# Optimization experiments

Measured on AMD Instinct MI355X. Metric: run time of the kernel, lower is better.

## Reference

```python
import jax, jax.numpy as jnp
import numpy as np

N = 128000      # total nodes
B = 128         # graphs, 1000 nodes each
L = 4           # max_levels
S_MAX = 1000    # max cluster size (<= PositionalEncoding max_len)
H = 128         # hidden dim (all conv output dims equal)
IN_DIM = 128
OUT_DIM = 1
E = 1024000
TEMP = 0.1


def layer_norm(x, g, b, eps=1e-5):
    mu = jnp.mean(x, axis=-1, keepdims=True)
    v = jnp.mean((x - mu) ** 2, axis=-1, keepdims=True)
    return (x - mu) * jax.lax.rsqrt(v + eps) * g + b


def transformer_conv(x, src, dst, Wq, bq, Wk, bk, Wv, bv, Ws, bs):
    # PyG TransformerConv, heads=1: softmax over in-edges of each dst node
    q = x @ Wq + bq
    k = x @ Wk + bk
    v = x @ Wv + bv
    logits = jnp.sum(q[dst] * k[src], axis=-1) / jnp.sqrt(jnp.float32(q.shape[-1]))
    m = jax.ops.segment_max(logits, dst, num_segments=N)
    e = jnp.exp(logits - m[dst])
    s = jax.ops.segment_sum(e, dst, num_segments=N)
    alpha = e / s[dst]
    agg = jax.ops.segment_sum(alpha[:, None] * v[src], dst, num_segments=N)
    return agg + x @ Ws + bs  # root_weight skip connection


def pos_encoding(S, d):
    pos = jnp.arange(S, dtype=jnp.float32)[:, None]
    div = jnp.exp(jnp.arange(0, d, 2, dtype=jnp.float32) * (-jnp.log(10000.0) / d))
    pe = jnp.zeros((S, d), jnp.float32)
    pe = pe.at[:, 0::2].set(jnp.sin(pos * div))
    pe = pe.at[:, 1::2].set(jnp.cos(pos * div))
    return pe


def gru(xseq, Wih, Whh, bih, bhh):
    # xseq: [G, S, H] -> outputs [G, S, H]; torch GRU gate math
    G = xseq.shape[0]
    def step(h, x_t):
        gi = x_t @ Wih.T + bih
        gh = h @ Whh.T + bhh
        ir, iz, inn = jnp.split(gi, 3, axis=-1)
        hr, hz, hn = jnp.split(gh, 3, axis=-1)
        r = jax.nn.sigmoid(ir + hr)
        z = jax.nn.sigmoid(iz + hz)
        n = jnp.tanh(inn + r * hn)
        h_new = (1.0 - z) * n + z * h
        return h_new, h_new
    h0 = jnp.zeros((G, Whh.shape[1]), xseq.dtype)
    _, outs = jax.lax.scan(step, h0, jnp.swapaxes(xseq, 0, 1))
    return jnp.swapaxes(outs, 0, 1)


def _forward(x, tree_edge_index, call_sequences, batch,
             conv_Wq, conv_bq, conv_Wk, conv_bk, conv_Wv, conv_bv, conv_Ws, conv_bs,
             ln_g, ln_b, centers, proj_W, proj_b,
             gru_Wih, gru_Whh, gru_bih, gru_bhh, seqln_g, seqln_b,
             lin1_W, lin1_b, lin2_W, lin2_b):
    src, dst = tree_edge_index[0], tree_edge_index[1]
    h = x
    for i in range(3):  # conv1/bn1, conv2/bn2, conv4/bn4
        h = transformer_conv(h, src, dst, conv_Wq[i], conv_bq[i], conv_Wk[i],
                             conv_bk[i], conv_Wv[i], conv_bv[i], conv_Ws[i], conv_bs[i])
        h = jax.nn.relu(layer_norm(h, ln_g[i], ln_b[i]))

    # HierarchicalClassifier: cosine-sim soft assignment + center variance loss
    xn = h / jnp.maximum(jnp.linalg.norm(h, axis=-1, keepdims=True), 1e-8)
    cn = centers / jnp.maximum(jnp.linalg.norm(centers, axis=-1, keepdims=True), 1e-8)
    assign = jax.nn.softmax((xn @ cn.T) / TEMP, axis=-1)
    level_ids = jnp.argmax(assign, axis=1).astype(jnp.int32)
    iu0, iu1 = np.triu_indices(L, k=1)
    dvec = jnp.linalg.norm(centers[iu0] - centers[iu1], axis=-1)
    distance = -jnp.var(dvec, ddof=1)  # torch.var is unbiased

    # ragged gather + pad: group nodes by (graph, cluster), sort by call order
    G = B * L
    group = batch * L + level_ids                       # [N]
    order = jnp.argsort(group * N + call_sequences)     # sort by group, then call
    g_sorted = group[order]
    counts = jax.ops.segment_sum(jnp.ones((N,), jnp.int32), group, num_segments=G)
    starts = jnp.cumsum(counts) - counts
    pos = jnp.arange(N, dtype=jnp.int32) - starts[g_sorted]
    seq = jnp.zeros((G, S_MAX, H), h.dtype).at[g_sorted, pos].set(h[order])

    # SequentialRNN: proj -> pos-enc -> GRU -> LayerNorm -> ReLU (mask unused)
    sin = seq @ proj_W + proj_b + pos_encoding(S_MAX, H)[None]
    outs = gru(sin, gru_Wih, gru_Whh, gru_bih, gru_bhh)
    outs = jax.nn.relu(layer_norm(outs, seqln_g, seqln_b))

    # scatter valid positions back; singleton clusters keep raw features
    node_out = jnp.zeros_like(h).at[order].set(outs[g_sorted, pos])
    singleton = (counts[group] == 1)
    gout = jnp.where(singleton[:, None], h, node_out)

    y = jax.nn.gelu(gout @ lin1_W + lin1_b, approximate=False)
    y = jax.nn.sigmoid(y @ lin2_W + lin2_b)
    return y, distance


def setup_inputs():
    key = jax.random.key(0)
    ks = jax.random.split(key, 16)
    p = lambda k, s: jax.random.normal(k, s, jnp.float32) * 0.02
    return {
        "x": jax.random.normal(ks[0], (N, IN_DIM), jnp.float32),
        "tree_edge_index": jax.random.randint(ks[1], (2, E), 0, N, dtype=jnp.int32),
        "call_sequences": jax.random.permutation(ks[2], N).astype(jnp.int32),
        "batch": (jnp.arange(N, dtype=jnp.int32) * B) // N,  # 1000 nodes per graph
        "conv_Wq": p(ks[3], (3, H, H)), "conv_bq": jnp.zeros((3, H), jnp.float32),
        "conv_Wk": p(ks[4], (3, H, H)), "conv_bk": jnp.zeros((3, H), jnp.float32),
        "conv_Wv": p(ks[5], (3, H, H)), "conv_bv": jnp.zeros((3, H), jnp.float32),
        "conv_Ws": p(ks[6], (3, H, H)), "conv_bs": jnp.zeros((3, H), jnp.float32),
        "ln_g": jnp.ones((3, H), jnp.float32), "ln_b": jnp.zeros((3, H), jnp.float32),
        "centers": jax.random.normal(ks[7], (L, H), jnp.float32),
        "proj_W": p(ks[8], (H, H)), "proj_b": jnp.zeros((H,), jnp.float32),
        "gru_Wih": p(ks[9], (3 * H, H)), "gru_Whh": p(ks[10], (3 * H, H)),
        "gru_bih": jnp.zeros((3 * H,), jnp.float32), "gru_bhh": jnp.zeros((3 * H,), jnp.float32),
        "seqln_g": jnp.ones((H,), jnp.float32), "seqln_b": jnp.zeros((H,), jnp.float32),
        "lin1_W": p(ks[11], (H, 8)), "lin1_b": jnp.zeros((8,), jnp.float32),
        "lin2_W": p(ks[12], (8, OUT_DIM)), "lin2_b": jnp.zeros((OUT_DIM,), jnp.float32),
    }


def reference(x, tree_edge_index, call_sequences, batch,
              conv_Wq, conv_bq, conv_Wk, conv_bk, conv_Wv, conv_bv, conv_Ws, conv_bs,
              ln_g, ln_b, centers, proj_W, proj_b,
              gru_Wih, gru_Whh, gru_bih, gru_bhh, seqln_g, seqln_b,
              lin1_W, lin1_b, lin2_W, lin2_b):
    return _forward(x, tree_edge_index, call_sequences, batch,
                    conv_Wq, conv_bq, conv_Wk, conv_bk, conv_Wv, conv_bv, conv_Ws, conv_bs,
                    ln_g, ln_b, centers, proj_W, proj_b,
                    gru_Wih, gru_Whh, gru_bih, gru_bhh, seqln_g, seqln_b,
                    lin1_W, lin1_b, lin2_W, lin2_b)
```

## Files before the change

kernel.cpp:

```cpp
#include <hip/hip_runtime.h>

#define NN 128000
#define EE 1024000
#define HH 128
#define GG 512
#define SMAX 1000
#define NCHUNK 500

typedef unsigned int u32;
typedef unsigned short u16;

constexpr size_t NH     = (size_t)NN*HH;
constexpr size_t F_H    = 0;
constexpr size_t F_A    = NH;
constexpr size_t F_B    = 2*NH;
constexpr size_t F_NODE = F_A + (size_t)NN*192;
constexpr size_t F_CN   = 3*NH;
constexpr size_t F_WKT  = F_CN   + 512;
constexpr size_t F_WQK  = F_WKT  + 3*16384;
constexpr size_t F_BQK  = F_WQK  + 3*16384;
constexpr size_t F_CW   = F_BQK  + 3*128;
constexpr size_t F_PEW  = F_CW   + 128*384;
constexpr size_t F_PEB  = F_PEW  + 1000*384;
constexpr size_t F_END  = F_PEB  + 1000*128;

constexpr size_t I_ROWP = 0;
constexpr size_t I_CUR  = I_ROWP + NN + 8;
constexpr size_t I_COL  = I_CUR  + NN;
constexpr size_t I_GRP  = I_COL  + EE;
constexpr size_t I_INV  = I_GRP  + NN;
constexpr size_t I_POS  = I_INV  + NN;
constexpr size_t I_GN   = I_POS  + NN;
constexpr size_t I_CNT  = I_GN   + (size_t)GG*SMAX;
constexpr size_t I_CH   = I_CNT  + GG;
constexpr size_t I_BS   = I_CH   + (size_t)NCHUNK*GG;
constexpr size_t I_WT   = I_BS   + 512;
constexpr size_t I_END  = I_WT   + 64*384;

constexpr size_t WS_NEEDED = F_END*4 + I_END*4;

__device__ inline float wredf(float v){
  #pragma unroll
  for (int o = 32; o; o >>= 1) v += __shfl_xor(v, o);
  return v;
}
__device__ inline u32 bf16rne(float f){
  u32 u = __float_as_uint(f);
  return (u + 0x7fffu + ((u >> 16) & 1u)) >> 16;
}
__device__ inline float bf2f(u16 u){
  return __uint_as_float(((u32)u) << 16);
}
__device__ inline float frcp(float x){
#if __has_builtin(__builtin_amdgcn_rcpf)
  return __builtin_amdgcn_rcpf(x);
#else
  return 1.f / x;
#endif
}

typedef _Float16 h2_t __attribute__((ext_vector_type(2)));
__device__ inline float dot2f(u32 w, u32 h, float acc){
#if __has_builtin(__builtin_amdgcn_fdot2)
  return __builtin_amdgcn_fdot2(__builtin_bit_cast(h2_t, w),
                                __builtin_bit_cast(h2_t, h), acc, false);
#else
  float r;
  asm("v_dot2_f32_f16 %0, %1, %2, %3" : "=v"(r) : "v"(w), "v"(h), "v"(acc));
  return r;
#endif
}
#define PIN4(v) asm volatile("" : "+v"((v).x), "+v"((v).y), "+v"((v).z), "+v"((v).w))

__global__ void k_sentinel(float* __restrict__ out, int n, float val){
  int i = blockIdx.x * 256 + threadIdx.x;
  if (i < n) out[i] = val;
}

__global__ void k_zero(int* __restrict__ p){
  p[blockIdx.x * 256 + threadIdx.x] = 0;
}
__global__ void k_hist(const int* __restrict__ dst, int* __restrict__ deg){
  int e = blockIdx.x * 256 + threadIdx.x;
  atomicAdd(&deg[dst[e]], 1);
}
__global__ void k_s1(const int* __restrict__ deg, int* __restrict__ bsum){
  __shared__ int red[256];
  int t = threadIdx.x;
  red[t] = deg[blockIdx.x * 256 + t];
  __syncthreads();
  for (int s = 128; s; s >>= 1){ if (t < s) red[t] += red[t + s]; __syncthreads(); }
  if (!t) bsum[blockIdx.x] = red[0];
}
__global__ void k_s2(int* __restrict__ bsum){
  __shared__ int arr[512];
  int t = threadIdx.x;
  int v0 = (t < NCHUNK) ? bsum[t] : 0;
  arr[t] = v0; __syncthreads();
  for (int off = 1; off < 512; off <<= 1){
    int v = (t >= off) ? arr[t - off] : 0;
    __syncthreads();
    arr[t] += v;
    __syncthreads();
  }
  if (t < NCHUNK) bsum[t] = arr[t] - v0;
}
__global__ void k_s3(const int* __restrict__ bsum, int* __restrict__ row_ptr,
                     int* __restrict__ cursor){
  __shared__ int arr[256];
  int t = threadIdx.x;
  int i = blockIdx.x * 256 + t;
  int v0 = cursor[i];
  arr[t] = v0; __syncthreads();
  for (int off = 1; off < 256; off <<= 1){
    int v = (t >= off) ? arr[t - off] : 0;
    __syncthreads();
    arr[t] += v;
    __syncthreads();
  }
  int exc = arr[t] - v0 + bsum[blockIdx.x];
  row_ptr[i] = exc;
  cursor[i]  = exc;
  if (i == 0) row_ptr[NN] = EE;
}
__global__ void k_scatter(const int* __restrict__ src, const int* __restrict__ dst,
                          int* __restrict__ cursor, int* __restrict__ col){
  int e = blockIdx.x * 256 + threadIdx.x;
  int idx = atomicAdd(&cursor[dst[e]], 1);
  col[idx] = src[e];
}

__global__ void k_setup(const float* __restrict__ centers, float* __restrict__ cn,
                        float* __restrict__ dist_out){
  __shared__ float red[128];
  int t = threadIdx.x;
  for (int l = 0; l < 4; ++l){
    float v = centers[l*128 + t];
    red[t] = v * v; __syncthreads();
    for (int s = 64; s; s >>= 1){ if (t < s) red[t] += red[t + s]; __syncthreads(); }
    float nrm = sqrtf(red[0]);
    __syncthreads();
    cn[l*128 + t] = v / fmaxf(nrm, 1e-8f);
  }
  const int iu0[6] = {0,0,0,1,1,2}, iu1[6] = {1,2,3,2,3,3};
  __shared__ float dv[6];
  for (int p = 0; p < 6; ++p){
    float d = centers[iu0[p]*128 + t] - centers[iu1[p]*128 + t];
    red[t] = d * d; __syncthreads();
    for (int s = 64; s; s >>= 1){ if (t < s) red[t] += red[t + s]; __syncthreads(); }
    if (!t) dv[p] = sqrtf(red[0]);
    __syncthreads();
  }
  if (!t){
    float mean = 0.f;
    for (int p = 0; p < 6; ++p) mean += dv[p];
    mean /= 6.f;
    float var = 0.f;
    for (int p = 0; p < 6; ++p){ float d = dv[p] - mean; var += d * d; }
    var /= 5.f;
    dist_out[0] = -var;
  }
}

__global__ void k_pe(const float* __restrict__ projb, float* __restrict__ peb){
  int p = blockIdx.x, t = threadIdx.x;
  float ex  = (float)(t >> 1) * (-2.0f * 9.210340371976184f / 128.0f);
  float ang = (float)p * expf(ex);
  float v = (t & 1) ? cosf(ang) : sinf(ang);
  peb[p*128 + t] = v + projb[t];
}
__global__ void k_pew(const float* __restrict__ peb, const float* __restrict__ Wih,
                      const float* __restrict__ bih, float* __restrict__ pew){
  int p = blockIdx.x;
  int j = blockIdx.y * 128 + threadIdx.x;
  const float* pb = peb + p*128;
  const float* wr = Wih + (size_t)j*128;
  float acc = bih[j];
  #pragma unroll 4
  for (int m = 0; m < 128; ++m) acc += pb[m] * wr[m];
  pew[(size_t)p*384 + j] = acc;
}
__global__ void k_combw(const float* __restrict__ projW, const float* __restrict__ Wih,
                        float* __restrict__ cw){
  int kk = blockIdx.x;
  int j  = blockIdx.y * 128 + threadIdx.x;
  const float* pr = projW + (size_t)kk*128;
  const float* wr = Wih + (size_t)j*128;
  float acc = 0.f;
  #pragma unroll 4
  for (int m = 0; m < 128; ++m) acc += pr[m] * wr[m];
  cw[(size_t)kk*384 + j] = acc;
}
__global__ void k_tr(const float* __restrict__ Wk, float* __restrict__ wkt){
  int kk = blockIdx.x, l = blockIdx.y, c = threadIdx.x;
  wkt[(size_t)l*16384 + kk*128 + c] = Wk[(size_t)l*16384 + c*128 + kk];
}
__global__ void k_mv(const float* __restrict__ M, const float* __restrict__ v,
                     float* __restrict__ out){
  int l = blockIdx.x, i = threadIdx.x;
  const float* row = M + (size_t)l*16384 + (size_t)i*128;
  const float* vv = v + l*128;
  float acc = 0.f;
  #pragma unroll 4
  for (int j = 0; j < 128; ++j) acc += row[j] * vv[j];
  out[l*128 + i] = acc;
}
__global__ void k_packwhh16(const float* __restrict__ Whh, u32* __restrict__ wt){
  int kp = blockIdx.x;
  int j  = blockIdx.y * 128 + threadIdx.x;
  _Float16 a = (_Float16)Whh[(size_t)j*128 + 2*kp];
  _Float16 b = (_Float16)Whh[(size_t)j*128 + 2*kp + 1];
  u32 lo = (u32)__builtin_bit_cast(u16, a);
  u32 hi = (u32)__builtin_bit_cast(u16, b);
  wt[(size_t)j*64 + kp] = (hi << 16) | lo;
}

__global__ __launch_bounds__(256, 2) void k_gemm(
    const float* __restrict__ X, const float* __restrict__ W, int ldw,
    const float* __restrict__ X2, const float* __restrict__ W2,
    const float* __restrict__ bias, const float* __restrict__ pew,
    const int* __restrict__ pos, float* __restrict__ out,
    u16* __restrict__ outb, int ldo,
    const float* __restrict__ lng, const float* __restrict__ lnb,
    const float* __restrict__ bvv, const int* __restrict__ rowp){
  __shared__ __align__(16) float Wl[64*132];
  __shared__ __align__(16) float Xl[64*132];
  int tid = threadIdx.x;
  int rb = blockIdx.x * 128;
  int cb = blockIdx.y * 128;
  int rg = tid >> 4;
  int cg = tid & 15;
  int kxor = (cg >> 2) & 3;
  float acc[8][8];
  #pragma unroll
  for (int a = 0; a < 8; ++a)
    #pragma unroll
    for (int b = 0; b < 8; ++b) acc[a][b] = 0.f;
  int nhalf = X2 ? 4 : 2;
  for (int half = 0; half < nhalf; ++half){
    const float* Xs = (half < 2) ? X : X2;
    const float* Ws = (half < 2) ? W : W2;
    int ldws = (half < 2) ? ldw : 128;
    int hk = half & 1;
    __syncthreads();
    #pragma unroll
    for (int it = 0; it < 8; ++it){
      int idx = it*256 + tid;
      int kk = idx >> 5, c4 = idx & 31;
      *(float4*)&Wl[kk*132 + c4*4] =
          *(const float4*)&Ws[(size_t)(hk*64 + kk)*ldws + cb + c4*4];
    }
    #pragma unroll
    for (int it = 0; it < 8; ++it){
      int idx = it*256 + tid;
      int r = idx >> 4, c4 = idx & 15;
      float4 xv = *(const float4*)&Xs[(size_t)(rb + r)*128 + hk*64 + c4*4];
      Xl[(c4*4+0)*132 + r] = xv.x;
      Xl[(c4*4+1)*132 + r] = xv.y;
      Xl[(c4*4+2)*132 + r] = xv.z;
      Xl[(c4*4+3)*132 + r] = xv.w;
    }
    __syncthreads();
    #pragma unroll 2
    for (int kk = 0; kk < 64; ++kk){
      int kx = kk ^ kxor;
      float4 wa = *(const float4*)&Wl[kx*132 + cg*8];
      float4 wb = *(const float4*)&Wl[kx*132 + cg*8 + 4];
      float4 xa = *(const float4*)&Xl[kx*132 + rg*8];
      float4 xb = *(const float4*)&Xl[kx*132 + rg*8 + 4];
      float xs[8] = {xa.x, xa.y, xa.z, xa.w, xb.x, xb.y, xb.z, xb.w};
      float ws[8] = {wa.x, wa.y, wa.z, wa.w, wb.x, wb.y, wb.z, wb.w};
      #pragma unroll
      for (int rr = 0; rr < 8; ++rr)
        #pragma unroll
        for (int j = 0; j < 8; ++j) acc[rr][j] += xs[rr] * ws[j];
    }
  }
  if (lng){
    float gv[8], bl[8], bb[8], vv[8];
    #pragma unroll
    for (int j = 0; j < 8; ++j){
      int c = cg*8 + j;
      gv[j] = lng[c]; bl[j] = lnb[c]; bb[j] = bias[c]; vv[j] = bvv[c];
    }
    #pragma unroll
    for (int rr = 0; rr < 8; ++rr){
      int r = rb + rg*8 + rr;
      bool deg = rowp[r+1] > rowp[r];
      float rs = 0.f, rq = 0.f;
      #pragma unroll
      for (int j = 0; j < 8; ++j){
        float v = acc[rr][j] + bb[j] + (deg ? vv[j] : 0.f);
        acc[rr][j] = v;
        rs += v; rq += v*v;
      }
      #pragma unroll
      for (int o = 8; o; o >>= 1){ rs += __shfl_xor(rs, o); rq += __shfl_xor(rq, o); }
      float mu = rs * 0.0078125f;
      float var = rq * 0.0078125f - mu*mu;
      float rstd = rsqrtf(var + 1e-5f);
      float ov[8];
      #pragma unroll
      for (int j = 0; j < 8; ++j)
        ov[j] = fmaxf((acc[rr][j] - mu)*rstd*gv[j] + bl[j], 0.f);
      float* op = out + (size_t)r*128 + cg*8;
      *(float4*)op       = *(const float4*)&ov[0];
      *(float4*)(op + 4) = *(const float4*)&ov[4];
    }
    return;
  }
  #pragma unroll
  for (int rr = 0; rr < 8; ++rr){
    int r = rb + rg*8 + rr;
    float bv[8];
    if (pos){
      const float* pw = pew + (size_t)pos[r]*384 + cb + cg*8;
      #pragma unroll
      for (int j = 0; j < 8; ++j) bv[j] = pw[j];
    } else if (bias){
      #pragma unroll
      for (int j = 0; j < 8; ++j) bv[j] = bias[cb + cg*8 + j];
    } else {
      #pragma unroll
      for (int j = 0; j < 8; ++j) bv[j] = 0.f;
    }
    if (outb){
      u16 ob[8];
      #pragma unroll
      for (int j = 0; j < 8; ++j) ob[j] = (u16)bf16rne(acc[rr][j] + bv[j]);
      *(uint4*)(outb + (size_t)r*ldo + cb + cg*8) = *(const uint4*)ob;
    } else {
      float ov[8];
      #pragma unroll
      for (int j = 0; j < 8; ++j) ov[j] = acc[rr][j] + bv[j];
      float* op = out + (size_t)r*ldo + cb + cg*8;
      *(float4*)op       = *(const float4*)&ov[0];
      *(float4*)(op + 4) = *(const float4*)&ov[4];
    }
  }
}

__global__ __launch_bounds__(256) void k_edge(
    const float* __restrict__ qt, const float* __restrict__ xsrc,
    const int* __restrict__ row_ptr, const int* __restrict__ col,
    float* __restrict__ xagg){
  int d = blockIdx.x * 8 + (threadIdx.x >> 5);
  int lane = threadIdx.x & 31;
  int e0 = row_ptr[d], e1 = row_ptr[d+1];
  if (e0 == e1){
    *(float4*)&xagg[(size_t)d*128 + lane*4] = make_float4(0.f, 0.f, 0.f, 0.f);
    return;
  }
  const float S = 0.08838834764831845f;
  float4 qv = *(const float4*)&qt[(size_t)d*128 + lane*4];
  float ss0 = 0.f, ss1 = 0.f;
  float4 A0 = make_float4(0.f,0.f,0.f,0.f), A1 = make_float4(0.f,0.f,0.f,0.f);
  int e = e0;
  for (; e + 1 < e1; e += 2){
    float4 x0 = *(const float4*)&xsrc[(size_t)col[e]  *128 + lane*4];
    float4 x1 = *(const float4*)&xsrc[(size_t)col[e+1]*128 + lane*4];
    float p0 = qv.x*x0.x + qv.y*x0.y + qv.z*x0.z + qv.w*x0.w;
    float p1 = qv.x*x1.x + qv.y*x1.y + qv.z*x1.z + qv.w*x1.w;
    #pragma unroll
    for (int o = 16; o; o >>= 1){ p0 += __shfl_xor(p0, o); p1 += __shfl_xor(p1, o); }
    float el0 = __expf(p0 * S);
    float el1 = __expf(p1 * S);
    ss0 += el0; ss1 += el1;
    A0.x += el0*x0.x; A0.y += el0*x0.y; A0.z += el0*x0.z; A0.w += el0*x0.w;
    A1.x += el1*x1.x; A1.y += el1*x1.y; A1.z += el1*x1.z; A1.w += el1*x1.w;
  }
  if (e < e1){
    float4 x0 = *(const float4*)&xsrc[(size_t)col[e]*128 + lane*4];
    float p0 = qv.x*x0.x + qv.y*x0.y + qv.z*x0.z + qv.w*x0.w;
    #pragma unroll
    for (int o = 16; o; o >>= 1) p0 += __shfl_xor(p0, o);
    float el0 = __expf(p0 * S);
    ss0 += el0;
    A0.x += el0*x0.x; A0.y += el0*x0.y; A0.z += el0*x0.z; A0.w += el0*x0.w;
  }
  float inv = 1.f / (ss0 + ss1);
  *(float4*)&xagg[(size_t)d*128 + lane*4] =
      make_float4((A0.x+A1.x)*inv, (A0.y+A1.y)*inv, (A0.z+A1.z)*inv, (A0.w+A1.w)*inv);
}

__global__ __launch_bounds__(256) void k_lnrelu_cls(
    const float* __restrict__ in, const float* __restrict__ g,
    const float* __restrict__ b, const float* __restrict__ bvv,
    const int* __restrict__ rowp, float* __restrict__ outp,
    const float* __restrict__ cn, const int* __restrict__ batch,
    const int* __restrict__ callsq, int* __restrict__ grp, int* __restrict__ inv){
  int node = blockIdx.x * 4 + (threadIdx.x >> 6);
  int lane = threadIdx.x & 63;
  float x0 = in[(size_t)node*128 + 2*lane], x1 = in[(size_t)node*128 + 2*lane + 1];
  if (rowp[node+1] > rowp[node]){
    x0 += bvv[2*lane];
    x1 += bvv[2*lane + 1];
  }
  float s = wredf(x0 + x1);
  float qq = wredf(x0*x0 + x1*x1);
  float mu = s * 0.0078125f;
  float var = qq * 0.0078125f - mu*mu;
  float rstd = rsqrtf(var + 1e-5f);
  float y0 = fmaxf((x0 - mu)*rstd*g[2*lane]   + b[2*lane],   0.f);
  float y1 = fmaxf((x1 - mu)*rstd*g[2*lane+1] + b[2*lane+1], 0.f);
  outp[(size_t)node*128 + 2*lane]     = y0;
  outp[(size_t)node*128 + 2*lane + 1] = y1;
  float p0 = y0*cn[      2*lane] + y1*cn[      2*lane+1];
  float p1 = y0*cn[128 + 2*lane] + y1*cn[128 + 2*lane+1];
  float p2 = y0*cn[256 + 2*lane] + y1*cn[256 + 2*lane+1];
  float p3 = y0*cn[384 + 2*lane] + y1*cn[384 + 2*lane+1];
  p0 = wredf(p0); p1 = wredf(p1); p2 = wredf(p2); p3 = wredf(p3);
  if (lane == 0){
    float best = p0; int bi = 0;
    if (p1 > best){ best = p1; bi = 1; }
    if (p2 > best){ best = p2; bi = 2; }
    if (p3 > best){ best = p3; bi = 3; }
    grp[node] = batch[node]*4 + bi;
    inv[callsq[node]] = node;
  }
}

__global__ __launch_bounds__(256) void k_g1(const int* __restrict__ inv,
                                            const int* __restrict__ grp,
                                            int* __restrict__ ch){
  __shared__ int hist[GG];
  int c = blockIdx.x, t = threadIdx.x;
  hist[t] = 0; hist[t + 256] = 0;
  __syncthreads();
  int g = grp[inv[c*256 + t]];
  atomicAdd(&hist[g], 1);
  __syncthreads();
  ch[c*GG + t] = hist[t];
  ch[c*GG + 256 + t] = hist[256 + t];
}
__global__ void k_g2(int* __restrict__ ch, int* __restrict__ cnt){
  __shared__ int arr[512];
  int g = blockIdx.x, t = threadIdx.x;
  int v0 = (t < NCHUNK) ? ch[(size_t)t*GG + g] : 0;
  arr[t] = v0; __syncthreads();
  for (int off = 1; off < 512; off <<= 1){
    int v = (t >= off) ? arr[t - off] : 0;
    __syncthreads();
    arr[t] += v;
    __syncthreads();
  }
  if (t < NCHUNK) ch[(size_t)t*GG + g] = arr[t] - v0;
  if (t == 511) cnt[g] = arr[511];
}
__global__ __launch_bounds__(256) void k_g3(
    const int* __restrict__ inv, const int* __restrict__ grp,
    const int* __restrict__ ch, int* __restrict__ pos, int* __restrict__ gn){
  __shared__ int hist[GG];
  int c = blockIdx.x, t = threadIdx.x;
  hist[t] = 0; hist[t + 256] = 0;
  __syncthreads();
  int node = inv[c*256 + t];
  int g = grp[node];
  int lane = t & 63, w = t >> 6;
  int before = 0, total = 0;
  for (int j = 0; j < 64; ++j){
    int gj = __shfl(g, j);
    if (gj == g){ total++; if (j < lane) before++; }
  }
  int base = 0;
  for (int wv = 0; wv < 4; ++wv){
    if (w == wv){
      base = hist[g];
      if (before == total - 1) hist[g] = base + total;
    }
    __syncthreads();
  }
  int p = ch[c*GG + g] + base + before;
  pos[node] = p;
  gn[(size_t)g*SMAX + p] = node;
}

#define GRU_STEP(XR, XZ, XN, NODE, CUR, NXT)                                     \
  {                                                                              \
    const uint4* HB = (const uint4*)&hb16[CUR][0];                               \
    uint4 hh[8];                                                                 \
    _Pragma("unroll")                                                            \
    for (int s = 0; s < 8; ++s) hh[s] = HB[kh*8 + s];                            \
    __builtin_amdgcn_s_setprio(1);                                               \
    float ar = 0.f, az = 0.f, an = 0.f;                                          \
    _Pragma("unroll")                                                            \
    for (int s = 0; s < 8; ++s){                                                 \
      ar = dot2f(wr_[s].x, hh[s].x, ar); az = dot2f(wz_[s].x, hh[s].x, az); an = dot2f(wn_[s].x, hh[s].x, an); \
      ar = dot2f(wr_[s].y, hh[s].y, ar); az = dot2f(wz_[s].y, hh[s].y, az); an = dot2f(wn_[s].y, hh[s].y, an); \
      ar = dot2f(wr_[s].z, hh[s].z, ar); az = dot2f(wz_[s].z, hh[s].z, az); an = dot2f(wn_[s].z, hh[s].z, an); \
      ar = dot2f(wr_[s].w, hh[s].w, ar); az = dot2f(wz_[s].w, hh[s].w, az); an = dot2f(wn_[s].w, hh[s].w, an); \
    }                                                                            \
    ar += __shfl_xor(ar, 1); az += __shfl_xor(az, 1); an += __shfl_xor(an, 1);   \
    ar += br; az += bz; an += bn;                                                \
    float er = __expf(-((XR) + ar));                                             \
    float rg_ = frcp(1.f + er);                                                  \
    float ez = __expf(-((XZ) + az));                                             \
    float zg_ = frcp(1.f + ez);                                                  \
    float yv = (XN) + rg_ * an;                                                  \
    float e2 = __expf(-2.f * yv);                                                \
    float ng_ = (1.f - e2) * frcp(1.f + e2);                                     \
    float hnew = ng_ + zg_ * (hprev - ng_);                                      \
    __builtin_amdgcn_s_setprio(0);                                               \
    hprev = hnew;                                                                \
    u16 hbf = (u16)bf16rne(hnew);                                                \
    u32 pk = ((u32)(u16)__shfl_xor((int)hbf, 2) << 16) | (u32)hbf;               \
    if (!kh){                                                                    \
      _Float16 hf16 = (_Float16)hnew;                                            \
      hb16[NXT][j] = __builtin_bit_cast(u16, hf16);                              \
    }                                                                            \
    if ((t & 3) == 0)                                                            \
      *(u32*)(node_out + (size_t)(NODE)*128 + j) = pk;                           \
    asm volatile("s_waitcnt lgkmcnt(0)" ::: "memory");                           \
    __builtin_amdgcn_s_barrier();                                                \
    asm volatile("" ::: "memory");                                               \
  }

__global__ __launch_bounds__(256)
__attribute__((amdgpu_waves_per_eu(2, 2)))
void k_gru(
    const u16* __restrict__ gi, const u32* __restrict__ wt,
    const float* __restrict__ bhh, const int* __restrict__ gn,
    const int* __restrict__ cnt, u16* __restrict__ node_out){
  __shared__ __align__(16) u16 hb16[2][128];
  int t = threadIdx.x;
  int j = t >> 1;
  int kh = t & 1;
  int g = blockIdx.x;
  int my = cnt[g];
  if (my <= 1) return;
  uint4 wr_[8], wz_[8], wn_[8];
  {
    const uint4* wt4 = (const uint4*)wt;
    size_t b0 = (size_t)(0*128 + j)*16 + kh*8;
    size_t b1 = (size_t)(1*128 + j)*16 + kh*8;
    size_t b2 = (size_t)(2*128 + j)*16 + kh*8;
    #pragma unroll
    for (int s = 0; s < 8; ++s){
      wr_[s] = wt4[b0 + s];
      wz_[s] = wt4[b1 + s];
      wn_[s] = wt4[b2 + s];
    }
    #pragma unroll
    for (int s = 0; s < 8; ++s){
      PIN4(wr_[s]); PIN4(wz_[s]); PIN4(wn_[s]);
    }
  }
  if (t < 128) hb16[0][t] = 0;
  float br = bhh[j], bz = bhh[128 + j], bn = bhh[256 + j];
  const int* gnr = gn + (size_t)g*SMAX;
  float hprev = 0.f;
  int n0 = gnr[0];
  int n1 = gnr[min(1, my - 1)];
  int n2 = gnr[min(2, my - 1)];
  int n3 = gnr[min(3, my - 1)];
  u16 a0r, a0z, a0n, a1r, a1z, a1n;
  u16 b0r, b0z, b0n, b1r, b1z, b1n;
  {
    const u16* g0 = gi + (size_t)n0*384;
    const u16* g1 = gi + (size_t)n1*384;
    a0r = g0[j]; a0z = g0[128 + j]; a0n = g0[256 + j];
    a1r = g1[j]; a1z = g1[128 + j]; a1n = g1[256 + j];
    const u16* g2 = gi + (size_t)n2*384;
    const u16* g3 = gi + (size_t)n3*384;
    b0r = g2[j]; b0z = g2[128 + j]; b0n = g2[256 + j];
    b1r = g3[j]; b1z = g3[128 + j]; b1n = g3[256 + j];
  }
  int nn0 = gnr[min(4, my - 1)];
  int nn1 = gnr[min(5, my - 1)];
  int nn2 = gnr[min(6, my - 1)];
  int nn3 = gnr[min(7, my - 1)];
  __syncthreads();
  int K = my >> 2;
  for (int k = 0; k < K; ++k){
    int base = k*4;
    int n4 = nn0, n5 = nn1, n6 = nn2, n7 = nn3;
    float x0r = bf2f(a0r), x0z = bf2f(a0z), x0n = bf2f(a0n);
    float x1r = bf2f(a1r), x1z = bf2f(a1z), x1n = bf2f(a1n);
    {
      const u16* g4 = gi + (size_t)n4*384;
      const u16* g5 = gi + (size_t)n5*384;
      a0r = g4[j]; a0z = g4[128 + j]; a0n = g4[256 + j];
      a1r = g5[j]; a1z = g5[128 + j]; a1n = g5[256 + j];
    }
    GRU_STEP(x0r, x0z, x0n, n0, 0, 1);
    GRU_STEP(x1r, x1z, x1n, n1, 1, 0);
    float x2r = bf2f(b0r), x2z = bf2f(b0z), x2n = bf2f(b0n);
    float x3r = bf2f(b1r), x3z = bf2f(b1z), x3n = bf2f(b1n);
    {
      const u16* g6 = gi + (size_t)n6*384;
      const u16* g7 = gi + (size_t)n7*384;
      b0r = g6[j]; b0z = g6[128 + j]; b0n = g6[256 + j];
      b1r = g7[j]; b1z = g7[128 + j]; b1n = g7[256 + j];
    }
    GRU_STEP(x2r, x2z, x2n, n2, 0, 1);
    GRU_STEP(x3r, x3z, x3n, n3, 1, 0);
    nn0 = gnr[min(base + 8,  my - 1)];
    nn1 = gnr[min(base + 9,  my - 1)];
    nn2 = gnr[min(base + 10, my - 1)];
    nn3 = gnr[min(base + 11, my - 1)];
    n0 = n4; n1 = n5; n2 = n6; n3 = n7;
  }
  for (int p = K*4; p < my; ++p){
    int node = gnr[p];
    const u16* gr = gi + (size_t)node*384;
    float xr = bf2f(gr[j]), xz = bf2f(gr[128 + j]), xn = bf2f(gr[256 + j]);
    int cur = p & 1, nxt = cur ^ 1;
    GRU_STEP(xr, xz, xn, node, cur, nxt);
  }
}

__global__ __launch_bounds__(256) void k_head(
    const float* __restrict__ h, const u16* __restrict__ node_out,
    const int* __restrict__ grp, const int* __restrict__ cnt,
    const float* __restrict__ sqg, const float* __restrict__ sqb,
    const float* __restrict__ l1W, const float* __restrict__ l1b,
    const float* __restrict__ l2W, const float* __restrict__ l2b,
    float* __restrict__ out){
  int node = blockIdx.x * 4 + (threadIdx.x >> 6);
  int lane = threadIdx.x & 63;
  bool single = (cnt[grp[node]] == 1);
  float x0, x1;
  if (single){
    x0 = h[(size_t)node*128 + 2*lane];
    x1 = h[(size_t)node*128 + 2*lane + 1];
  } else {
    float r0 = bf2f(node_out[(size_t)node*128 + 2*lane]);
    float r1 = bf2f(node_out[(size_t)node*128 + 2*lane + 1]);
    float s = wredf(r0 + r1);
    float qq = wredf(r0*r0 + r1*r1);
    float mu = s * 0.0078125f;
    float var = qq * 0.0078125f - mu*mu;
    float rstd = rsqrtf(var + 1e-5f);
    x0 = fmaxf((r0 - mu)*rstd*sqg[2*lane]   + sqb[2*lane],   0.f);
    x1 = fmaxf((r1 - mu)*rstd*sqg[2*lane+1] + sqb[2*lane+1], 0.f);
  }
  float acc[8];
  #pragma unroll
  for (int j = 0; j < 8; ++j)
    acc[j] = x0 * l1W[(2*lane)*8 + j] + x1 * l1W[(2*lane + 1)*8 + j];
  #pragma unroll
  for (int o = 32; o; o >>= 1)
    #pragma unroll
    for (int j = 0; j < 8; ++j) acc[j] += __shfl_xor(acc[j], o);
  if (lane == 0){
    float zz = l2b[0];
    #pragma unroll
    for (int j = 0; j < 8; ++j){
      float xx = acc[j] + l1b[j];
      float ge = 0.5f * xx * (1.f + erff(xx * 0.7071067811865476f));
      zz += ge * l2W[j];
    }
    out[node] = 1.f / (1.f + expf(-zz));
  }
}

extern "C" void kernel_launch(void* const* d_in, const int* in_sizes, int n_in,
                              void* d_out, int out_size, void* d_ws, size_t ws_size,
                              hipStream_t stream){
  float* out = (float*)d_out;

  if (ws_size < WS_NEEDED){
    float code = -(float)(ws_size >> 20);
    k_sentinel<<<(out_size + 255)/256, 256, 0, stream>>>(out, out_size, code);
    return;
  }

  const float* x       = (const float*)d_in[0];
  const int*   tei     = (const int*)d_in[1];
  const int*   callsq  = (const int*)d_in[2];
  const int*   batch   = (const int*)d_in[3];
  const float* Wq      = (const float*)d_in[4];
  const float* bq      = (const float*)d_in[5];
  const float* Wk      = (const float*)d_in[6];
  const float* bk      = (const float*)d_in[7];
  const float* Wv      = (const float*)d_in[8];
  const float* bv      = (const float*)d_in[9];
  const float* Wsk     = (const float*)d_in[10];
  const float* bsk     = (const float*)d_in[11];
  const float* lng     = (const float*)d_in[12];
  const float* lnb     = (const float*)d_in[13];
  const float* centers = (const float*)d_in[14];
  const float* projW   = (const float*)d_in[15];
  const float* projb   = (const float*)d_in[16];
  const float* Wih     = (const float*)d_in[17];
  const float* Whh     = (const float*)d_in[18];
  const float* bih     = (const float*)d_in[19];
  const float* bhh     = (const float*)d_in[20];
  const float* sqg     = (const float*)d_in[21];
  const float* sqb     = (const float*)d_in[22];
  const float* l1W     = (const float*)d_in[23];
  const float* l1b     = (const float*)d_in[24];
  const float* l2W     = (const float*)d_in[25];
  const float* l2b     = (const float*)d_in[26];

  float* wf = (float*)d_ws;
  float* f_h    = wf + F_H;
  float* f_a    = wf + F_A;
  float* f_b    = wf + F_B;
  float* f_cn   = wf + F_CN;
  float* f_wkt  = wf + F_WKT;
  float* f_wqk  = wf + F_WQK;
  float* f_bqk  = wf + F_BQK;
  float* f_cw   = wf + F_CW;
  float* f_pew  = wf + F_PEW;
  float* f_peb  = wf + F_PEB;
  u16*   gi_bf  = (u16*)(wf + F_A);
  u16*   no_bf  = (u16*)(wf + F_NODE);
  int* wi = (int*)(wf + F_END);
  int* i_rowp = wi + I_ROWP;
  int* i_cur  = wi + I_CUR;
  int* i_col  = wi + I_COL;
  int* i_grp  = wi + I_GRP;
  int* i_inv  = wi + I_INV;
  int* i_pos  = wi + I_POS;
  int* i_gn   = wi + I_GN;
  int* i_cnt  = wi + I_CNT;
  int* i_ch   = wi + I_CH;
  int* i_bs   = wi + I_BS;
  u32* i_wt   = (u32*)(wi + I_WT);

  const int* esrc = tei;
  const int* edst = tei + EE;

  k_zero<<<NN/256, 256, 0, stream>>>(i_cur);
  k_hist<<<EE/256, 256, 0, stream>>>(edst, i_cur);
  k_s1<<<NCHUNK, 256, 0, stream>>>(i_cur, i_bs);
  k_s2<<<1, 512, 0, stream>>>(i_bs);
  k_s3<<<NCHUNK, 256, 0, stream>>>(i_bs, i_rowp, i_cur);
  k_scatter<<<EE/256, 256, 0, stream>>>(esrc, edst, i_cur, i_col);

  k_setup<<<1, 128, 0, stream>>>(centers, f_cn, out + NN);
  k_pe<<<1000, 128, 0, stream>>>(projb, f_peb);
  k_pew<<<dim3(1000, 3), 128, 0, stream>>>(f_peb, Wih, bih, f_pew);
  k_tr<<<dim3(128, 3), 128, 0, stream>>>(Wk, f_wkt);
  for (int i = 0; i < 3; ++i)
    k_gemm<<<dim3(1, 1), 256, 0, stream>>>(Wq + (size_t)i*16384, f_wkt + (size_t)i*16384,
        128, nullptr, nullptr, nullptr, nullptr, nullptr, f_wqk + (size_t)i*16384,
        nullptr, 128, nullptr, nullptr, nullptr, nullptr);
  k_mv<<<3, 128, 0, stream>>>(Wk, bq, f_bqk);
  k_combw<<<dim3(128, 3), 128, 0, stream>>>(projW, Wih, f_cw);
  k_packwhh16<<<dim3(64, 3), 128, 0, stream>>>(Whh, i_wt);

  for (int i = 0; i < 3; ++i){
    const float* xin = i ? f_h : x;
    size_t wo = (size_t)i * 128 * 128, bo = (size_t)i * 128;
    k_gemm<<<dim3(NN/128, 1), 256, 0, stream>>>(xin, f_wqk + (size_t)i*16384, 128,
        nullptr, nullptr, f_bqk + bo, nullptr, nullptr, f_b, nullptr, 128,
        nullptr, nullptr, nullptr, nullptr);
    k_edge<<<NN/8, 256, 0, stream>>>(f_b, xin, i_rowp, i_col, f_a);
    if (i < 2){
      k_gemm<<<dim3(NN/128, 1), 256, 0, stream>>>(f_a, Wv + wo, 128, xin, Wsk + wo,
          bsk + bo, nullptr, nullptr, f_h, nullptr, 128,
          lng + bo, lnb + bo, bv + bo, i_rowp);
    } else {
      k_gemm<<<dim3(NN/128, 1), 256, 0, stream>>>(f_a, Wv + wo, 128, xin, Wsk + wo,
          bsk + bo, nullptr, nullptr, f_b, nullptr, 128,
          nullptr, nullptr, nullptr, nullptr);
      k_lnrelu_cls<<<NN/4, 256, 0, stream>>>(f_b, lng + bo, lnb + bo, bv + bo, i_rowp,
          f_h, f_cn, batch, callsq, i_grp, i_inv);
    }
  }

  k_g1<<<NCHUNK, 256, 0, stream>>>(i_inv, i_grp, i_ch);
  k_g2<<<GG, 512, 0, stream>>>(i_ch, i_cnt);
  k_g3<<<NCHUNK, 256, 0, stream>>>(i_inv, i_grp, i_ch, i_pos, i_gn);

  k_gemm<<<dim3(NN/128, 3), 256, 0, stream>>>(f_h, f_cw, 384, nullptr, nullptr,
      nullptr, f_pew, i_pos, nullptr, gi_bf, 384, nullptr, nullptr, nullptr, nullptr);

  k_gru<<<GG, 256, 0, stream>>>(gi_bf, i_wt, bhh, i_gn, i_cnt, no_bf);

  k_head<<<NN/4, 256, 0, stream>>>(f_h, no_bf, i_grp, i_cnt, sqg, sqb,
                                   l1W, l1b, l2W, l2b, out);
}
```

Baseline: 2.091 ms.

## Scatter GRU input rows into cluster-contiguous order and simplify GRU prefetch

Adds a prefix scan over cluster counts and a per-node destination row, so the input-projection GEMM writes its bf16 gate inputs straight into cluster-sequential order. The GRU kernel then reads consecutive rows instead of chasing node indices, which removes the dependent gather from the serial recurrence, and its prefetch shrinks from 4-deep to 2-deep. The node output store also changes from a shuffle-packed 32-bit write to a per-lane 16-bit write. The GEMM epilogue now does scattered row stores, and the shallower prefetch may expose more load latency in the serial loop.

```diff
diff --git a/kernel.cpp b/kernel.cpp
--- a/kernel.cpp
+++ b/kernel.cpp
@@ -35,7 +35,9 @@
 constexpr size_t I_CH   = I_CNT  + GG;
 constexpr size_t I_BS   = I_CH   + (size_t)NCHUNK*GG;
 constexpr size_t I_WT   = I_BS   + 512;
-constexpr size_t I_END  = I_WT   + 64*384;
+constexpr size_t I_DST  = I_WT   + 64*384;
+constexpr size_t I_STARTS = I_DST + NN;
+constexpr size_t I_END  = I_STARTS + 512;
 
 constexpr size_t WS_NEEDED = F_END*4 + I_END*4;
 
@@ -222,7 +224,8 @@
     const int* __restrict__ pos, float* __restrict__ out,
     u16* __restrict__ outb, int ldo,
     const float* __restrict__ lng, const float* __restrict__ lnb,
-    const float* __restrict__ bvv, const int* __restrict__ rowp){
+    const float* __restrict__ bvv, const int* __restrict__ rowp,
+    const int* __restrict__ dstrow){
   __shared__ __align__(16) float Wl[64*132];
   __shared__ __align__(16) float Xl[64*132];
   int tid = threadIdx.x;
@@ -324,16 +327,17 @@
       #pragma unroll
       for (int j = 0; j < 8; ++j) bv[j] = 0.f;
     }
+    int orow = dstrow ? dstrow[r] : r;
     if (outb){
       u16 ob[8];
       #pragma unroll
       for (int j = 0; j < 8; ++j) ob[j] = (u16)bf16rne(acc[rr][j] + bv[j]);
-      *(uint4*)(outb + (size_t)r*ldo + cb + cg*8) = *(const uint4*)ob;
+      *(uint4*)(outb + (size_t)orow*ldo + cb + cg*8) = *(const uint4*)ob;
     } else {
       float ov[8];
       #pragma unroll
       for (int j = 0; j < 8; ++j) ov[j] = acc[rr][j] + bv[j];
-      float* op = out + (size_t)r*ldo + cb + cg*8;
+      float* op = out + (size_t)orow*ldo + cb + cg*8;
       *(float4*)op       = *(const float4*)&ov[0];
       *(float4*)(op + 4) = *(const float4*)&ov[4];
     }
@@ -447,9 +451,23 @@
   if (t < NCHUNK) ch[(size_t)t*GG + g] = arr[t] - v0;
   if (t == 511) cnt[g] = arr[511];
 }
+__global__ void k_g4(const int* __restrict__ cnt, int* __restrict__ starts){
+  __shared__ int arr[512];
+  int t = threadIdx.x;
+  int v0 = cnt[t];
+  arr[t] = v0; __syncthreads();
+  for (int off = 1; off < 512; off <<= 1){
+    int v = (t >= off) ? arr[t - off] : 0;
+    __syncthreads();
+    arr[t] += v;
+    __syncthreads();
+  }
+  starts[t] = arr[t] - v0;
+}
 __global__ __launch_bounds__(256) void k_g3(
     const int* __restrict__ inv, const int* __restrict__ grp,
-    const int* __restrict__ ch, int* __restrict__ pos, int* __restrict__ gn){
+    const int* __restrict__ ch, const int* __restrict__ starts,
+    int* __restrict__ pos, int* __restrict__ dst, int* __restrict__ gn){
   __shared__ int hist[GG];
   int c = blockIdx.x, t = threadIdx.x;
   hist[t] = 0; hist[t + 256] = 0;
@@ -472,6 +490,7 @@
   }
   int p = ch[c*GG + g] + base + before;
   pos[node] = p;
+  dst[node] = starts[g] + p;
   gn[(size_t)g*SMAX + p] = node;
 }
 
@@ -502,14 +521,11 @@
     float hnew = ng_ + zg_ * (hprev - ng_);                                      \
     __builtin_amdgcn_s_setprio(0);                                               \
     hprev = hnew;                                                                \
-    u16 hbf = (u16)bf16rne(hnew);                                                \
-    u32 pk = ((u32)(u16)__shfl_xor((int)hbf, 2) << 16) | (u32)hbf;               \
     if (!kh){                                                                    \
       _Float16 hf16 = (_Float16)hnew;                                            \
       hb16[NXT][j] = __builtin_bit_cast(u16, hf16);                              \
+      node_out[(size_t)(NODE)*128 + j] = (u16)bf16rne(hnew);                     \
     }                                                                            \
-    if ((t & 3) == 0)                                                            \
-      *(u32*)(node_out + (size_t)(NODE)*128 + j) = pk;                           \
     asm volatile("s_waitcnt lgkmcnt(0)" ::: "memory");                           \
     __builtin_amdgcn_s_barrier();                                                \
     asm volatile("" ::: "memory");                                               \
@@ -520,7 +536,8 @@
 void k_gru(
     const u16* __restrict__ gi, const u32* __restrict__ wt,
     const float* __restrict__ bhh, const int* __restrict__ gn,
-    const int* __restrict__ cnt, u16* __restrict__ node_out){
+    const int* __restrict__ cnt, const int* __restrict__ starts,
+    u16* __restrict__ node_out){
   __shared__ __align__(16) u16 hb16[2][128];
   int t = threadIdx.x;
   int j = t >> 1;
@@ -548,64 +565,32 @@
   if (t < 128) hb16[0][t] = 0;
   float br = bhh[j], bz = bhh[128 + j], bn = bhh[256 + j];
   const int* gnr = gn + (size_t)g*SMAX;
+  const u16* grow = gi + (size_t)starts[g]*384;
   float hprev = 0.f;
-  int n0 = gnr[0];
-  int n1 = gnr[min(1, my - 1)];
-  int n2 = gnr[min(2, my - 1)];
-  int n3 = gnr[min(3, my - 1)];
-  u16 a0r, a0z, a0n, a1r, a1z, a1n;
-  u16 b0r, b0z, b0n, b1r, b1z, b1n;
-  {
-    const u16* g0 = gi + (size_t)n0*384;
-    const u16* g1 = gi + (size_t)n1*384;
-    a0r = g0[j]; a0z = g0[128 + j]; a0n = g0[256 + j];
-    a1r = g1[j]; a1z = g1[128 + j]; a1n = g1[256 + j];
-    const u16* g2 = gi + (size_t)n2*384;
-    const u16* g3 = gi + (size_t)n3*384;
-    b0r = g2[j]; b0z = g2[128 + j]; b0n = g2[256 + j];
-    b1r = g3[j]; b1z = g3[128 + j]; b1n = g3[256 + j];
-  }
-  int nn0 = gnr[min(4, my - 1)];
-  int nn1 = gnr[min(5, my - 1)];
-  int nn2 = gnr[min(6, my - 1)];
-  int nn3 = gnr[min(7, my - 1)];
+  u16 a_r = grow[j], a_z = grow[128 + j], a_n = grow[256 + j];
+  const u16* g1r = grow + (size_t)min(1, my - 1)*384;
+  u16 b_r = g1r[j], b_z = g1r[128 + j], b_n = g1r[256 + j];
+  int nodeA = gnr[0];
+  int nodeB = gnr[min(1, my - 1)];
   __syncthreads();
-  int K = my >> 2;
-  for (int k = 0; k < K; ++k){
-    int base = k*4;
-    int n4 = nn0, n5 = nn1, n6 = nn2, n7 = nn3;
-    float x0r = bf2f(a0r), x0z = bf2f(a0z), x0n = bf2f(a0n);
-    float x1r = bf2f(a1r), x1z = bf2f(a1z), x1n = bf2f(a1n);
+  for (int p = 0; p < my; p += 2){
+    float xr = bf2f(a_r), xz = bf2f(a_z), xn = bf2f(a_n);
+    int nA = nodeA;
     {
-      const u16* g4 = gi + (size_t)n4*384;
-      const u16* g5 = gi + (size_t)n5*384;
-      a0r = g4[j]; a0z = g4[128 + j]; a0n = g4[256 + j];
-      a1r = g5[j]; a1z = g5[128 + j]; a1n = g5[256 + j];
-    }
-    GRU_STEP(x0r, x0z, x0n, n0, 0, 1);
-    GRU_STEP(x1r, x1z, x1n, n1, 1, 0);
-    float x2r = bf2f(b0r), x2z = bf2f(b0z), x2n = bf2f(b0n);
-    float x3r = bf2f(b1r), x3z = bf2f(b1z), x3n = bf2f(b1n);
+      const u16* g2r = grow + (size_t)min(p + 2, my - 1)*384;
+      a_r = g2r[j]; a_z = g2r[128 + j]; a_n = g2r[256 + j];
+      nodeA = gnr[min(p + 2, my - 1)];
+    }
+    GRU_STEP(xr, xz, xn, nA, 0, 1);
+    if (p + 1 >= my) break;
+    float yr = bf2f(b_r), yz = bf2f(b_z), yn = bf2f(b_n);
+    int nB = nodeB;
     {
-      const u16* g6 = gi + (size_t)n6*384;
-      const u16* g7 = gi + (size_t)n7*384;
-      b0r = g6[j]; b0z = g6[128 + j]; b0n = g6[256 + j];
-      b1r = g7[j]; b1z = g7[128 + j]; b1n = g7[256 + j];
-    }
-    GRU_STEP(x2r, x2z, x2n, n2, 0, 1);
-    GRU_STEP(x3r, x3z, x3n, n3, 1, 0);
-    nn0 = gnr[min(base + 8,  my - 1)];
-    nn1 = gnr[min(base + 9,  my - 1)];
-    nn2 = gnr[min(base + 10, my - 1)];
-    nn3 = gnr[min(base + 11, my - 1)];
-    n0 = n4; n1 = n5; n2 = n6; n3 = n7;
-  }
-  for (int p = K*4; p < my; ++p){
-    int node = gnr[p];
-    const u16* gr = gi + (size_t)node*384;
-    float xr = bf2f(gr[j]), xz = bf2f(gr[128 + j]), xn = bf2f(gr[256 + j]);
-    int cur = p & 1, nxt = cur ^ 1;
-    GRU_STEP(xr, xz, xn, node, cur, nxt);
+      const u16* g3r = grow + (size_t)min(p + 3, my - 1)*384;
+      b_r = g3r[j]; b_z = g3r[128 + j]; b_n = g3r[256 + j];
+      nodeB = gnr[min(p + 3, my - 1)];
+    }
+    GRU_STEP(yr, yz, yn, nB, 1, 0);
   }
 }
 
@@ -718,6 +703,8 @@
   int* i_ch   = wi + I_CH;
   int* i_bs   = wi + I_BS;
   u32* i_wt   = (u32*)(wi + I_WT);
+  int* i_dst  = wi + I_DST;
+  int* i_st   = wi + I_STARTS;
 
   const int* esrc = tei;
   const int* edst = tei + EE;
@@ -736,7 +723,7 @@
   for (int i = 0; i < 3; ++i)
     k_gemm<<<dim3(1, 1), 256, 0, stream>>>(Wq + (size_t)i*16384, f_wkt + (size_t)i*16384,
         128, nullptr, nullptr, nullptr, nullptr, nullptr, f_wqk + (size_t)i*16384,
-        nullptr, 128, nullptr, nullptr, nullptr, nullptr);
+        nullptr, 128, nullptr, nullptr, nullptr, nullptr, nullptr);
   k_mv<<<3, 128, 0, stream>>>(Wk, bq, f_bqk);
   k_combw<<<dim3(128, 3), 128, 0, stream>>>(projW, Wih, f_cw);
   k_packwhh16<<<dim3(64, 3), 128, 0, stream>>>(Whh, i_wt);
@@ -746,16 +733,16 @@
     size_t wo = (size_t)i * 128 * 128, bo = (size_t)i * 128;
     k_gemm<<<dim3(NN/128, 1), 256, 0, stream>>>(xin, f_wqk + (size_t)i*16384, 128,
         nullptr, nullptr, f_bqk + bo, nullptr, nullptr, f_b, nullptr, 128,
-        nullptr, nullptr, nullptr, nullptr);
+        nullptr, nullptr, nullptr, nullptr, nullptr);
     k_edge<<<NN/8, 256, 0, stream>>>(f_b, xin, i_rowp, i_col, f_a);
     if (i < 2){
       k_gemm<<<dim3(NN/128, 1), 256, 0, stream>>>(f_a, Wv + wo, 128, xin, Wsk + wo,
           bsk + bo, nullptr, nullptr, f_h, nullptr, 128,
-          lng + bo, lnb + bo, bv + bo, i_rowp);
+          lng + bo, lnb + bo, bv + bo, i_rowp, nullptr);
     } else {
       k_gemm<<<dim3(NN/128, 1), 256, 0, stream>>>(f_a, Wv + wo, 128, xin, Wsk + wo,
           bsk + bo, nullptr, nullptr, f_b, nullptr, 128,
-          nullptr, nullptr, nullptr, nullptr);
+          nullptr, nullptr, nullptr, nullptr, nullptr);
       k_lnrelu_cls<<<NN/4, 256, 0, stream>>>(f_b, lng + bo, lnb + bo, bv + bo, i_rowp,
           f_h, f_cn, batch, callsq, i_grp, i_inv);
     }
@@ -763,12 +750,14 @@
 
   k_g1<<<NCHUNK, 256, 0, stream>>>(i_inv, i_grp, i_ch);
   k_g2<<<GG, 512, 0, stream>>>(i_ch, i_cnt);
-  k_g3<<<NCHUNK, 256, 0, stream>>>(i_inv, i_grp, i_ch, i_pos, i_gn);
+  k_g4<<<1, 512, 0, stream>>>(i_cnt, i_st);
+  k_g3<<<NCHUNK, 256, 0, stream>>>(i_inv, i_grp, i_ch, i_st, i_pos, i_dst, i_gn);
 
   k_gemm<<<dim3(NN/128, 3), 256, 0, stream>>>(f_h, f_cw, 384, nullptr, nullptr,
-      nullptr, f_pew, i_pos, nullptr, gi_bf, 384, nullptr, nullptr, nullptr, nullptr);
-
-  k_gru<<<GG, 256, 0, stream>>>(gi_bf, i_wt, bhh, i_gn, i_cnt, no_bf);
+      nullptr, f_pew, i_pos, nullptr, gi_bf, 384, nullptr, nullptr, nullptr, nullptr,
+      i_dst);
+
+  k_gru<<<GG, 256, 0, stream>>>(gi_bf, i_wt, bhh, i_gn, i_cnt, i_st, no_bf);
 
   k_head<<<NN/4, 256, 0, stream>>>(f_h, no_bf, i_grp, i_cnt, sqg, sqb,
                                    l1W, l1b, l2W, l2b, out);
```

Result: no change. 2.063 ms (-1.3%).
